# Performance work log

Measured on AMD Instinct MI355X. Metric: run time of the kernel, lower is better.

The kernel has to match this reference:

```python
import jax, jax.numpy as jnp
import numpy as np

NUM_HEADS = 8
T = 8  # hardcoded temporal dim in the original forward
MD = 3  # max_displacement -> 7x7 window
EPS = 1e-12  # F.normalize eps


def l2_normalize(x, axis):
    n = jnp.sqrt(jnp.sum(x * x, axis=axis, keepdims=True))
    return x / jnp.maximum(n, EPS)


def correlation_7x7(q, k):
    # q, k: [B, C, H, W]; FlowNet-style correlation, kernel_size=1, max_disp=3.
    # out[b, u, v, h, w] = sum_c q[b,c,h,w] * k[b,c,h+u-3,w+v-3] (zero padded)
    B, C, H, W = q.shape
    kp = jnp.pad(k, ((0, 0), (0, 0), (MD, MD), (MD, MD)))
    outs = []
    for dy in range(2 * MD + 1):
        for dx in range(2 * MD + 1):
            ks = kp[:, :, dy:dy + H, dx:dx + W]
            outs.append(jnp.sum(q * ks, axis=1))  # [B, H, W]
    corr = jnp.stack(outs, axis=1)  # [B, 49, H, W]
    return corr.reshape(B, 2 * MD + 1, 2 * MD + 1, H, W)


def setup_inputs() -> dict:
    key = jax.random.key(0)
    ks = jax.random.split(key, 6)
    B, N, C = 8, 8192, 256
    hd = C // NUM_HEADS
    std = 0.02
    return {
        "x": jax.random.normal(ks[0], (B, N, C), dtype=jnp.float32),
        "w_qk": jax.random.normal(ks[1], (2 * C, C), dtype=jnp.float32) * std,
        "w_corr": jax.random.normal(ks[2], (hd, 49), dtype=jnp.float32) * std,
        "b_corr": jnp.zeros((hd,), dtype=jnp.float32),
        "w_proj": jax.random.normal(ks[3], (C, C), dtype=jnp.float32) * std,
        "b_proj": jnp.zeros((C,), dtype=jnp.float32),
    }


def reference(x, w_qk, w_corr, b_corr, w_proj, b_proj):
    B, N, C = x.shape
    nh = NUM_HEADS
    hd = C // nh
    H = int(np.sqrt(N // T))
    W = H

    # qk projection (no bias): [B, N, 2C] -> q, k each [B, nh, N, hd]
    qk = jnp.einsum('bnc,dc->bnd', x, w_qk)
    qk = qk.reshape(B, N, 2, nh, hd).transpose(2, 0, 3, 1, 4)
    q, k = qk[0], qk[1]

    # 'b n (t h w) d -> (b n) t d h w'
    q = q.reshape(B * nh, T, H, W, hd).transpose(0, 1, 4, 2, 3)
    k = k.reshape(B * nh, T, H, W, hd).transpose(0, 1, 4, 2, 3)

    # temporal postfix: k[t+1], last frame repeated
    k_post = jnp.concatenate([k[:, 1:], k[:, -1:]], axis=1)

    qp = q.reshape(B * nh * T, hd, H, W)
    kp = k_post.reshape(B * nh * T, hd, H, W)
    qp = l2_normalize(qp, axis=1)
    kp = l2_normalize(kp, axis=1)

    corr = correlation_7x7(qp, kp)  # [(B nh T), 7, 7, H, W]
    # 'b u v h w -> b (h w) (u v)'
    corr = corr.transpose(0, 3, 4, 1, 2).reshape(B * nh * T, H * W, 49)

    v = jnp.einsum('bpk,dk->bpd', corr, w_corr) + b_corr  # [(B nh T), HW, hd]

    # '(b n t) (h w) d -> b n (t h w) d' then 'b h n d -> b n (h d)'
    out = v.reshape(B, nh, T * H * W, hd).transpose(0, 2, 1, 3).reshape(B, N, C)
    out = jnp.einsum('bnc,dc->bnd', out, w_proj) + b_proj
    return out
```

## Files before the change

### kernel.cpp

```cpp
#include <hip/hip_runtime.h>

typedef _Float16 half8 __attribute__((ext_vector_type(8)));
typedef _Float16 half2v __attribute__((ext_vector_type(2)));
typedef float float4v __attribute__((ext_vector_type(4)));

__device__ __forceinline__ float dot2acc(unsigned a, unsigned b, float c) {
#if __has_builtin(__builtin_amdgcn_fdot2)
  return __builtin_amdgcn_fdot2(__builtin_bit_cast(half2v, a), __builtin_bit_cast(half2v, b), c, false);
#else
  half2v ha = __builtin_bit_cast(half2v, a);
  half2v hb = __builtin_bit_cast(half2v, b);
  c += (float)ha[0] * (float)hb[0];
  c += (float)ha[1] * (float)hb[1];
  return c;
#endif
}
__device__ __forceinline__ unsigned hscale(unsigned a, float s) {
  half2v ha = __builtin_bit_cast(half2v, a);
  half2v r;
  r[0] = (_Float16)((float)ha[0] * s);
  r[1] = (_Float16)((float)ha[1] * s);
  return __builtin_bit_cast(unsigned, r);
}
__device__ __forceinline__ void gload_lds16(const void* g, void* l) {
  __builtin_amdgcn_global_load_lds((const __attribute__((address_space(1))) unsigned*)g,
                                   (__attribute__((address_space(3))) unsigned*)l, 16, 0, 0);
}
__device__ __forceinline__ unsigned short h2u(float v) {
  _Float16 h = (_Float16)v;
  return __builtin_bit_cast(unsigned short, h);
}

__global__ void cvt_all(const float4* __restrict__ x, const float4* __restrict__ wqk,
                        const float4* __restrict__ wpj,
                        ushort4* __restrict__ x16, ushort4* __restrict__ wqk16,
                        ushort4* __restrict__ wpj16) {
  int b = blockIdx.x;
  const float4* s;
  ushort4* d;
  int i;
  if (b < 16384) { s = x; d = x16; i = b * 256 + threadIdx.x; }
  else if (b < 16512) { s = wqk; d = wqk16; i = (b - 16384) * 256 + threadIdx.x; }
  else { s = wpj; d = wpj16; i = (b - 16512) * 256 + threadIdx.x; }
  float4 v = s[i];
  ushort4 o;
  o.x = h2u(v.x); o.y = h2u(v.y); o.z = h2u(v.z); o.w = h2u(v.w);
  d[i] = o;
}

__global__ __launch_bounds__(256, 2)
void gemm_qk(const _Float16* __restrict__ A, const _Float16* __restrict__ Bw,
             _Float16* __restrict__ qo, _Float16* __restrict__ ko) {
  __shared__ _Float16 Ash[4096];
  __shared__ _Float16 Bsh[4096];
  const int tid = threadIdx.x;
  const int lane = tid & 63, w = tid >> 6;
  const int wm = w >> 1, wn = w & 1;
  const int ml = lane & 15, qd = lane >> 4;
  const int m0 = blockIdx.y * 128, n0 = blockIdx.x * 128;

  float4v acc[4][4];
  float4v z = {0.f, 0.f, 0.f, 0.f};
#pragma unroll
  for (int i = 0; i < 4; ++i)
#pragma unroll
    for (int j = 0; j < 4; ++j) acc[i][j] = z;

  const _Float16* Ap = A + (size_t)m0 * 256;
  const _Float16* Bp = Bw + (size_t)n0 * 256;
  const int gr = w * 64 + lane;
  const int row0 = gr >> 2, kb = gr & 3;

  for (int kt = 0; kt < 8; ++kt) {
    int k0 = kt * 32;
    gload_lds16(Ap + row0 * 256 + k0 + kb * 8, Ash + (size_t)(w * 64) * 8);
    gload_lds16(Ap + (row0 + 64) * 256 + k0 + kb * 8, Ash + (size_t)(256 + w * 64) * 8);
    gload_lds16(Bp + row0 * 256 + k0 + kb * 8, Bsh + (size_t)(w * 64) * 8);
    gload_lds16(Bp + (row0 + 64) * 256 + k0 + kb * 8, Bsh + (size_t)(256 + w * 64) * 8);
    __syncthreads();
    half8 af[4], bf[4];
#pragma unroll
    for (int im = 0; im < 4; ++im) {
      af[im] = *(const half8*)(Ash + (wm * 64 + im * 16 + ml) * 32 + qd * 8);
      bf[im] = *(const half8*)(Bsh + (wn * 64 + im * 16 + ml) * 32 + qd * 8);
    }
#pragma unroll
    for (int im = 0; im < 4; ++im)
#pragma unroll
      for (int in = 0; in < 4; ++in)
        acc[im][in] = __builtin_amdgcn_mfma_f32_16x16x32_f16(bf[in], af[im], acc[im][in], 0, 0, 0);
    __syncthreads();
  }

#pragma unroll
  for (int im = 0; im < 4; ++im) {
    int rowr = m0 + wm * 64 + im * 16 + ml;
    int b = rowr >> 13, nn = rowr & 8191;
    int t = nn >> 10, yx = nn & 1023;
#pragma unroll
    for (int in = 0; in < 4; ++in) {
      int nc0 = n0 + wn * 64 + in * 16 + qd * 4;
      int s = nc0 >> 8, h = (nc0 >> 5) & 7, j0 = nc0 & 31;
      _Float16* dst = s ? ko : qo;
      ushort4 pk;
      pk.x = h2u(acc[im][in][0]);
      pk.y = h2u(acc[im][in][1]);
      pk.z = h2u(acc[im][in][2]);
      pk.w = h2u(acc[im][in][3]);
      int p = b * 64 + h * 8 + t;
      *(ushort4*)(dst + ((size_t)p * 1024 + yx) * 32 + j0) = pk;
    }
  }
}

__global__ __launch_bounds__(256, 4)
void corr_kernel(const _Float16* __restrict__ q16, const _Float16* __restrict__ k16,
                 const float* __restrict__ wcorr, const float* __restrict__ bcorr,
                 _Float16* __restrict__ outp) {
  __shared__ uint4 smem[2304];
  __shared__ uint4 wcs[256];

  const int tid = threadIdx.x;
  const int bx = blockIdx.x;
  const int p = bx >> 2, tile = bx & 3;
  const int y0 = (tile >> 1) * 16, x0 = (tile & 1) * 16;
  const int b = p >> 6, h = (p >> 3) & 7, t = p & 7;
  const int pk = (t < 7) ? p + 1 : p;
  const int ty = tid >> 4, tx = tid & 15;

  _Float16* wch = (_Float16*)wcs;
  for (int idx = tid; idx < 2048; idx += 256) {
    int d = idx >> 6, kk = idx & 63;
    float v = (kk < 49) ? wcorr[d * 49 + kk] : (kk == 49 ? bcorr[d] : 0.f);
    wch[idx] = (_Float16)v;
  }

  const _Float16* kbase = k16 + (size_t)pk * 32768;
#pragma unroll
  for (int i = 0; i < 8; ++i) {
    int g = tid + i * 256;
    if (g < 1936) {
      int vec = g >> 2, part = g & 3;
      int ky = vec / 22, kx = vec - ky * 22;
      int gy = y0 + ky - 3, gx = x0 + kx - 3;
      uint4 val = make_uint4(0u, 0u, 0u, 0u);
      if (gy >= 0 && gy < 32 && gx >= 0 && gx < 32)
        val = *(const uint4*)(kbase + ((size_t)gy * 32 + gx) * 32 + part * 8);
      smem[part * 485 + vec] = val;
    }
  }
  __syncthreads();

  for (int v = tid; v < 484; v += 256) {
    uint4 gg[4];
#pragma unroll
    for (int pq = 0; pq < 4; ++pq) gg[pq] = smem[pq * 485 + v];
    float ss = 0.f;
#pragma unroll
    for (int pq = 0; pq < 4; ++pq) {
      const unsigned* u = (const unsigned*)&gg[pq];
#pragma unroll
      for (int e = 0; e < 4; ++e) ss = dot2acc(u[e], u[e], ss);
    }
    float sc = 1.f / fmaxf(sqrtf(ss), 1e-12f);
#pragma unroll
    for (int pq = 0; pq < 4; ++pq) {
      unsigned* u = (unsigned*)&gg[pq];
#pragma unroll
      for (int e = 0; e < 4; ++e) u[e] = hscale(u[e], sc);
      smem[pq * 485 + v] = gg[pq];
    }
  }
  __syncthreads();

  const _Float16* qptr = q16 + (size_t)p * 32768 + ((size_t)(y0 + ty) * 32 + (x0 + tx)) * 32;
  uint4 qv[4];
#pragma unroll
  for (int i = 0; i < 4; ++i) qv[i] = *(const uint4*)(qptr + i * 8);
  unsigned* qu = (unsigned*)qv;
  float qss = 0.f;
#pragma unroll
  for (int e = 0; e < 16; ++e) qss = dot2acc(qu[e], qu[e], qss);
  float qsc = 1.f / fmaxf(sqrtf(qss), 1e-12f);
#pragma unroll
  for (int e = 0; e < 16; ++e) qu[e] = hscale(qu[e], qsc);

  const uint4* kwin = smem + (ty * 22 + tx);
  float corr[49];
#pragma unroll
  for (int i = 0; i < 49; ++i) corr[i] = 0.f;
#pragma unroll
  for (int pq = 0; pq < 4; ++pq) {
#pragma unroll
    for (int dy = 0; dy < 7; ++dy) {
#pragma unroll
      for (int dx = 0; dx < 7; ++dx) {
        uint4 kk = kwin[pq * 485 + dy * 22 + dx];
        const unsigned* ku = (const unsigned*)&kk;
        float c = corr[dy * 7 + dx];
        c = dot2acc(qu[pq * 4 + 0], ku[0], c);
        c = dot2acc(qu[pq * 4 + 1], ku[1], c);
        c = dot2acc(qu[pq * 4 + 2], ku[2], c);
        c = dot2acc(qu[pq * 4 + 3], ku[3], c);
        corr[dy * 7 + dx] = c;
      }
    }
  }
  __syncthreads();

#pragma unroll
  for (int i = 0; i < 8; ++i) {
    uint4 val;
    unsigned* vu = (unsigned*)&val;
#pragma unroll
    for (int e = 0; e < 4; ++e) {
      int idx = i * 8 + e * 2;
      half2v hh;
      hh[0] = (_Float16)(idx < 49 ? corr[idx] : (idx == 49 ? 1.f : 0.f));
      hh[1] = (_Float16)(idx + 1 < 49 ? corr[idx + 1] : (idx + 1 == 49 ? 1.f : 0.f));
      vu[e] = __builtin_bit_cast(unsigned, hh);
    }
    smem[tid * 9 + i] = val;
  }
  __syncthreads();

  _Float16* corrm = (_Float16*)smem;
  const int lane = tid & 63, w = tid >> 6;
  const int ml = lane & 15, qd = lane >> 4;
  float4v vacc[4][2];
  float4v z = {0.f, 0.f, 0.f, 0.f};
#pragma unroll
  for (int im = 0; im < 4; ++im) { vacc[im][0] = z; vacc[im][1] = z; }
#pragma unroll
  for (int ks = 0; ks < 2; ++ks) {
    half8 bfrag[2];
#pragma unroll
    for (int nt = 0; nt < 2; ++nt)
      bfrag[nt] = *(const half8*)(wch + (nt * 16 + ml) * 64 + ks * 32 + qd * 8);
#pragma unroll
    for (int im = 0; im < 4; ++im) {
      half8 afrag = *(const half8*)(corrm + (w * 64 + im * 16 + ml) * 72 + ks * 32 + qd * 8);
#pragma unroll
      for (int nt = 0; nt < 2; ++nt)
        vacc[im][nt] = __builtin_amdgcn_mfma_f32_16x16x32_f16(bfrag[nt], afrag, vacc[im][nt], 0, 0, 0);
    }
  }

#pragma unroll
  for (int im = 0; im < 4; ++im) {
    int pos = w * 64 + im * 16 + ml;
    int py = pos >> 4, px = pos & 15;
    int n = t * 1024 + (y0 + py) * 32 + (x0 + px);
#pragma unroll
    for (int nt = 0; nt < 2; ++nt) {
      int d0 = nt * 16 + qd * 4;
      ushort4 pkv;
      pkv.x = h2u(vacc[im][nt][0]);
      pkv.y = h2u(vacc[im][nt][1]);
      pkv.z = h2u(vacc[im][nt][2]);
      pkv.w = h2u(vacc[im][nt][3]);
      *(ushort4*)(outp + (((size_t)b * 8192 + n) << 8) + h * 32 + d0) = pkv;
    }
  }
}

__global__ __launch_bounds__(256, 2)
void gemm_proj(const _Float16* __restrict__ A, const _Float16* __restrict__ Bw,
               const float* __restrict__ bp, float* __restrict__ out) {
  __shared__ _Float16 Ash[4096];
  __shared__ _Float16 Bsh[4096];
  const int tid = threadIdx.x;
  const int lane = tid & 63, w = tid >> 6;
  const int wm = w >> 1, wn = w & 1;
  const int ml = lane & 15, qd = lane >> 4;
  const int m0 = blockIdx.y * 128, n0 = blockIdx.x * 128;

  float4v acc[4][4];
  float4v z = {0.f, 0.f, 0.f, 0.f};
#pragma unroll
  for (int i = 0; i < 4; ++i)
#pragma unroll
    for (int j = 0; j < 4; ++j) acc[i][j] = z;

  const _Float16* Ap = A + (size_t)m0 * 256;
  const _Float16* Bp = Bw + (size_t)n0 * 256;
  const int gr = w * 64 + lane;
  const int row0 = gr >> 2, kb = gr & 3;

  for (int kt = 0; kt < 8; ++kt) {
    int k0 = kt * 32;
    gload_lds16(Ap + row0 * 256 + k0 + kb * 8, Ash + (size_t)(w * 64) * 8);
    gload_lds16(Ap + (row0 + 64) * 256 + k0 + kb * 8, Ash + (size_t)(256 + w * 64) * 8);
    gload_lds16(Bp + row0 * 256 + k0 + kb * 8, Bsh + (size_t)(w * 64) * 8);
    gload_lds16(Bp + (row0 + 64) * 256 + k0 + kb * 8, Bsh + (size_t)(256 + w * 64) * 8);
    __syncthreads();
    half8 af[4], bf[4];
#pragma unroll
    for (int im = 0; im < 4; ++im) {
      af[im] = *(const half8*)(Ash + (wm * 64 + im * 16 + ml) * 32 + qd * 8);
      bf[im] = *(const half8*)(Bsh + (wn * 64 + im * 16 + ml) * 32 + qd * 8);
    }
#pragma unroll
    for (int im = 0; im < 4; ++im)
#pragma unroll
      for (int in = 0; in < 4; ++in)
        acc[im][in] = __builtin_amdgcn_mfma_f32_16x16x32_f16(bf[in], af[im], acc[im][in], 0, 0, 0);
    __syncthreads();
  }

#pragma unroll
  for (int im = 0; im < 4; ++im) {
    int rowr = m0 + wm * 64 + im * 16 + ml;
#pragma unroll
    for (int in = 0; in < 4; ++in) {
      int nc0 = n0 + wn * 64 + in * 16 + qd * 4;
      float4 bias = *(const float4*)(bp + nc0);
      float4 v;
      v.x = acc[im][in][0] + bias.x;
      v.y = acc[im][in][1] + bias.y;
      v.z = acc[im][in][2] + bias.z;
      v.w = acc[im][in][3] + bias.w;
      *(float4*)(out + (size_t)rowr * 256 + nc0) = v;
    }
  }
}

extern "C" void kernel_launch(void* const* d_in, const int* in_sizes, int n_in,
                              void* d_out, int out_size, void* d_ws, size_t ws_size,
                              hipStream_t stream) {
  const float* x      = (const float*)d_in[0];
  const float* w_qk   = (const float*)d_in[1];
  const float* w_corr = (const float*)d_in[2];
  const float* b_corr = (const float*)d_in[3];
  const float* w_proj = (const float*)d_in[4];
  const float* b_proj = (const float*)d_in[5];
  float* out = (float*)d_out;

  char* ws = (char*)d_ws;
  _Float16* x16   = (_Float16*)(ws);
  _Float16* q16   = (_Float16*)(ws + 33554432);
  _Float16* k16   = (_Float16*)(ws + 67108864);
  _Float16* op16  = (_Float16*)(ws + 100663296);
  _Float16* wqk16 = (_Float16*)(ws + 134217728);
  _Float16* wpj16 = (_Float16*)(ws + 134479872);

  cvt_all<<<16576, 256, 0, stream>>>((const float4*)x, (const float4*)w_qk, (const float4*)w_proj,
                                     (ushort4*)x16, (ushort4*)wqk16, (ushort4*)wpj16);
  gemm_qk<<<dim3(4, 512), 256, 0, stream>>>(x16, wqk16, q16, k16);
  corr_kernel<<<2048, 256, 0, stream>>>(q16, k16, w_corr, b_corr, op16);
  gemm_proj<<<dim3(2, 512), 256, 0, stream>>>(op16, wpj16, b_proj, out);
}
```

Measured before the change: 235.2 us.

## Compute two adjacent pixels per thread in correlation kernel with padded LDS

The correlation kernel now runs 128 threads per block, and each thread computes two horizontally adjacent output pixels. Each loaded K window vector is shared between the two 7x7 accumulators, which roughly halves LDS reads per correlation. The LDS row stride is padded from 22 to 23 to reduce bank conflicts, and the MFMA stage gives each wave 128 rows. Launch bounds on both GEMMs are raised to 4 blocks per CU. In exchange, the roughly 98 float accumulators per thread raise register pressure and may cause spills or lower occupancy.

```diff
diff --git a/kernel.cpp b/kernel.cpp
--- a/kernel.cpp
+++ b/kernel.cpp
@@ -48,7 +48,7 @@
   d[i] = o;
 }
 
-__global__ __launch_bounds__(256, 2)
+__global__ __launch_bounds__(256, 4)
 void gemm_qk(const _Float16* __restrict__ A, const _Float16* __restrict__ Bw,
              _Float16* __restrict__ qo, _Float16* __restrict__ ko) {
   __shared__ _Float16 Ash[4096];
@@ -113,7 +113,7 @@
   }
 }
 
-__global__ __launch_bounds__(256, 4)
+__global__ __launch_bounds__(128, 2)
 void corr_kernel(const _Float16* __restrict__ q16, const _Float16* __restrict__ k16,
                  const float* __restrict__ wcorr, const float* __restrict__ bcorr,
                  _Float16* __restrict__ outp) {
@@ -126,10 +126,11 @@
   const int y0 = (tile >> 1) * 16, x0 = (tile & 1) * 16;
   const int b = p >> 6, h = (p >> 3) & 7, t = p & 7;
   const int pk = (t < 7) ? p + 1 : p;
-  const int ty = tid >> 4, tx = tid & 15;
+  const int y = tid >> 3;
+  const int xb = (tid & 7) * 2;
 
   _Float16* wch = (_Float16*)wcs;
-  for (int idx = tid; idx < 2048; idx += 256) {
+  for (int idx = tid; idx < 2048; idx += 128) {
     int d = idx >> 6, kk = idx & 63;
     float v = (kk < 49) ? wcorr[d * 49 + kk] : (kk == 49 ? bcorr[d] : 0.f);
     wch[idx] = (_Float16)v;
@@ -137,8 +138,8 @@
 
   const _Float16* kbase = k16 + (size_t)pk * 32768;
 #pragma unroll
-  for (int i = 0; i < 8; ++i) {
-    int g = tid + i * 256;
+  for (int i = 0; i < 16; ++i) {
+    int g = tid + i * 128;
     if (g < 1936) {
       int vec = g >> 2, part = g & 3;
       int ky = vec / 22, kx = vec - ky * 22;
@@ -146,15 +147,17 @@
       uint4 val = make_uint4(0u, 0u, 0u, 0u);
       if (gy >= 0 && gy < 32 && gx >= 0 && gx < 32)
         val = *(const uint4*)(kbase + ((size_t)gy * 32 + gx) * 32 + part * 8);
-      smem[part * 485 + vec] = val;
+      smem[part * 507 + ky * 23 + kx] = val;
     }
   }
   __syncthreads();
 
-  for (int v = tid; v < 484; v += 256) {
+  for (int v = tid; v < 484; v += 128) {
+    int row = v / 22, col = v - row * 22;
+    int s0 = row * 23 + col;
     uint4 gg[4];
 #pragma unroll
-    for (int pq = 0; pq < 4; ++pq) gg[pq] = smem[pq * 485 + v];
+    for (int pq = 0; pq < 4; ++pq) gg[pq] = smem[pq * 507 + s0];
     float ss = 0.f;
 #pragma unroll
     for (int pq = 0; pq < 4; ++pq) {
@@ -168,69 +171,87 @@
       unsigned* u = (unsigned*)&gg[pq];
 #pragma unroll
       for (int e = 0; e < 4; ++e) u[e] = hscale(u[e], sc);
-      smem[pq * 485 + v] = gg[pq];
+      smem[pq * 507 + s0] = gg[pq];
     }
   }
   __syncthreads();
 
-  const _Float16* qptr = q16 + (size_t)p * 32768 + ((size_t)(y0 + ty) * 32 + (x0 + tx)) * 32;
-  uint4 qv[4];
-#pragma unroll
-  for (int i = 0; i < 4; ++i) qv[i] = *(const uint4*)(qptr + i * 8);
-  unsigned* qu = (unsigned*)qv;
-  float qss = 0.f;
-#pragma unroll
-  for (int e = 0; e < 16; ++e) qss = dot2acc(qu[e], qu[e], qss);
-  float qsc = 1.f / fmaxf(sqrtf(qss), 1e-12f);
-#pragma unroll
-  for (int e = 0; e < 16; ++e) qu[e] = hscale(qu[e], qsc);
-
-  const uint4* kwin = smem + (ty * 22 + tx);
-  float corr[49];
-#pragma unroll
-  for (int i = 0; i < 49; ++i) corr[i] = 0.f;
+  const _Float16* qptr = q16 + (size_t)p * 32768 + ((size_t)(y0 + y) * 32 + (x0 + xb)) * 32;
+  uint4 qv0[4], qv1[4];
+#pragma unroll
+  for (int i = 0; i < 4; ++i) { qv0[i] = *(const uint4*)(qptr + i * 8); qv1[i] = *(const uint4*)(qptr + 32 + i * 8); }
+  unsigned* qu0 = (unsigned*)qv0;
+  unsigned* qu1 = (unsigned*)qv1;
+  float qs0 = 0.f, qs1 = 0.f;
+#pragma unroll
+  for (int e = 0; e < 16; ++e) { qs0 = dot2acc(qu0[e], qu0[e], qs0); qs1 = dot2acc(qu1[e], qu1[e], qs1); }
+  float qc0 = 1.f / fmaxf(sqrtf(qs0), 1e-12f);
+  float qc1 = 1.f / fmaxf(sqrtf(qs1), 1e-12f);
+#pragma unroll
+  for (int e = 0; e < 16; ++e) { qu0[e] = hscale(qu0[e], qc0); qu1[e] = hscale(qu1[e], qc1); }
+
+  const uint4* kwin = smem + (y * 23 + xb);
+  float acc0[49], acc1[49];
+#pragma unroll
+  for (int i = 0; i < 49; ++i) { acc0[i] = 0.f; acc1[i] = 0.f; }
 #pragma unroll
   for (int pq = 0; pq < 4; ++pq) {
 #pragma unroll
     for (int dy = 0; dy < 7; ++dy) {
 #pragma unroll
-      for (int dx = 0; dx < 7; ++dx) {
-        uint4 kk = kwin[pq * 485 + dy * 22 + dx];
+      for (int c = 0; c < 8; ++c) {
+        uint4 kk = kwin[pq * 507 + dy * 23 + c];
         const unsigned* ku = (const unsigned*)&kk;
-        float c = corr[dy * 7 + dx];
-        c = dot2acc(qu[pq * 4 + 0], ku[0], c);
-        c = dot2acc(qu[pq * 4 + 1], ku[1], c);
-        c = dot2acc(qu[pq * 4 + 2], ku[2], c);
-        c = dot2acc(qu[pq * 4 + 3], ku[3], c);
-        corr[dy * 7 + dx] = c;
+        if (c < 7) {
+          float cc = acc0[dy * 7 + c];
+          cc = dot2acc(qu0[pq * 4 + 0], ku[0], cc);
+          cc = dot2acc(qu0[pq * 4 + 1], ku[1], cc);
+          cc = dot2acc(qu0[pq * 4 + 2], ku[2], cc);
+          cc = dot2acc(qu0[pq * 4 + 3], ku[3], cc);
+          acc0[dy * 7 + c] = cc;
+        }
+        if (c > 0) {
+          float cc = acc1[dy * 7 + c - 1];
+          cc = dot2acc(qu1[pq * 4 + 0], ku[0], cc);
+          cc = dot2acc(qu1[pq * 4 + 1], ku[1], cc);
+          cc = dot2acc(qu1[pq * 4 + 2], ku[2], cc);
+          cc = dot2acc(qu1[pq * 4 + 3], ku[3], cc);
+          acc1[dy * 7 + c - 1] = cc;
+        }
       }
     }
   }
   __syncthreads();
 
+  int pos0 = y * 16 + xb;
 #pragma unroll
   for (int i = 0; i < 8; ++i) {
-    uint4 val;
-    unsigned* vu = (unsigned*)&val;
+    uint4 v0, v1;
+    unsigned* u0 = (unsigned*)&v0;
+    unsigned* u1 = (unsigned*)&v1;
 #pragma unroll
     for (int e = 0; e < 4; ++e) {
       int idx = i * 8 + e * 2;
-      half2v hh;
-      hh[0] = (_Float16)(idx < 49 ? corr[idx] : (idx == 49 ? 1.f : 0.f));
-      hh[1] = (_Float16)(idx + 1 < 49 ? corr[idx + 1] : (idx + 1 == 49 ? 1.f : 0.f));
-      vu[e] = __builtin_bit_cast(unsigned, hh);
-    }
-    smem[tid * 9 + i] = val;
+      half2v h0, h1;
+      h0[0] = (_Float16)(idx < 49 ? acc0[idx] : (idx == 49 ? 1.f : 0.f));
+      h0[1] = (_Float16)(idx + 1 < 49 ? acc0[idx + 1] : (idx + 1 == 49 ? 1.f : 0.f));
+      h1[0] = (_Float16)(idx < 49 ? acc1[idx] : (idx == 49 ? 1.f : 0.f));
+      h1[1] = (_Float16)(idx + 1 < 49 ? acc1[idx + 1] : (idx + 1 == 49 ? 1.f : 0.f));
+      u0[e] = __builtin_bit_cast(unsigned, h0);
+      u1[e] = __builtin_bit_cast(unsigned, h1);
+    }
+    smem[pos0 * 9 + i] = v0;
+    smem[(pos0 + 1) * 9 + i] = v1;
   }
   __syncthreads();
 
   _Float16* corrm = (_Float16*)smem;
   const int lane = tid & 63, w = tid >> 6;
   const int ml = lane & 15, qd = lane >> 4;
-  float4v vacc[4][2];
+  float4v vacc[8][2];
   float4v z = {0.f, 0.f, 0.f, 0.f};
 #pragma unroll
-  for (int im = 0; im < 4; ++im) { vacc[im][0] = z; vacc[im][1] = z; }
+  for (int im = 0; im < 8; ++im) { vacc[im][0] = z; vacc[im][1] = z; }
 #pragma unroll
   for (int ks = 0; ks < 2; ++ks) {
     half8 bfrag[2];
@@ -238,8 +259,8 @@
     for (int nt = 0; nt < 2; ++nt)
       bfrag[nt] = *(const half8*)(wch + (nt * 16 + ml) * 64 + ks * 32 + qd * 8);
 #pragma unroll
-    for (int im = 0; im < 4; ++im) {
-      half8 afrag = *(const half8*)(corrm + (w * 64 + im * 16 + ml) * 72 + ks * 32 + qd * 8);
+    for (int im = 0; im < 8; ++im) {
+      half8 afrag = *(const half8*)(corrm + (w * 128 + im * 16 + ml) * 72 + ks * 32 + qd * 8);
 #pragma unroll
       for (int nt = 0; nt < 2; ++nt)
         vacc[im][nt] = __builtin_amdgcn_mfma_f32_16x16x32_f16(bfrag[nt], afrag, vacc[im][nt], 0, 0, 0);
@@ -247,8 +268,8 @@
   }
 
 #pragma unroll
-  for (int im = 0; im < 4; ++im) {
-    int pos = w * 64 + im * 16 + ml;
+  for (int im = 0; im < 8; ++im) {
+    int pos = w * 128 + im * 16 + ml;
     int py = pos >> 4, px = pos & 15;
     int n = t * 1024 + (y0 + py) * 32 + (x0 + px);
 #pragma unroll
@@ -264,7 +285,7 @@
   }
 }
 
-__global__ __launch_bounds__(256, 2)
+__global__ __launch_bounds__(256, 4)
 void gemm_proj(const _Float16* __restrict__ A, const _Float16* __restrict__ Bw,
                const float* __restrict__ bp, float* __restrict__ out) {
   __shared__ _Float16 Ash[4096];
@@ -347,6 +368,6 @@
   cvt_all<<<16576, 256, 0, stream>>>((const float4*)x, (const float4*)w_qk, (const float4*)w_proj,
                                      (ushort4*)x16, (ushort4*)wqk16, (ushort4*)wpj16);
   gemm_qk<<<dim3(4, 512), 256, 0, stream>>>(x16, wqk16, q16, k16);
-  corr_kernel<<<2048, 256, 0, stream>>>(q16, k16, w_corr, b_corr, op16);
+  corr_kernel<<<2048, 128, 0, stream>>>(q16, k16, w_corr, b_corr, op16);
   gemm_proj<<<dim3(2, 512), 256, 0, stream>>>(op16, wpj16, b_proj, out);
 }
```

Result: slower. 254.5 us (+8.2%).
